# Kernel tuning notes

Hardware: AMD Instinct MI355X
Metric: run time of the kernel (lower is better)

The kernel has to match this reference:

```python
import jax, jax.numpy as jnp
import numpy as np

N_HEAD = 16
ROPE_CACHE = 2500  # Rotary module caches tables of length 2500
NEG_INF = -1e30


def _rope_tables(head_dim):
    inv_freq = 1.0 / (10000.0 ** (jnp.arange(0, head_dim, 2, dtype=jnp.float32) / head_dim))
    t = jnp.arange(ROPE_CACHE, dtype=jnp.float32)
    freqs = t[:, None] * inv_freq[None, :]            # (2500, head_dim//2)
    emb = jnp.concatenate([freqs, freqs], axis=-1)    # (2500, head_dim)
    return jnp.cos(emb), jnp.sin(emb)


def _rotate_half(x):
    h = x.shape[-1] // 2
    return jnp.concatenate([-x[..., h:], x[..., :h]], axis=-1)


def setup_inputs() -> dict:
    key = jax.random.key(0)
    ks = jax.random.split(key, 8)
    B, S, D = 2, 2048, 1024
    H = N_HEAD
    hd = D // H
    return {
        "qx": jax.random.normal(ks[0], (B, S, D), jnp.float32),
        "kvx": jax.random.normal(ks[1], (B, S, D), jnp.float32),
        "k_cache": jnp.zeros((B, H, S, hd), jnp.float32),
        "v_cache": jnp.zeros((B, H, S, hd), jnp.float32),
        "Wq": jax.random.normal(ks[2], (D, D), jnp.float32) * 0.02,
        "bq": jnp.zeros((D,), jnp.float32),
        "Wk": jax.random.normal(ks[3], (D, D), jnp.float32) * 0.02,
        "Wv": jax.random.normal(ks[4], (D, D), jnp.float32) * 0.02,
        "bv": jnp.zeros((D,), jnp.float32),
        "Wo": jax.random.normal(ks[5], (D, D), jnp.float32) * 0.02,
        "bo": jnp.zeros((D,), jnp.float32),
        "q_positions": jnp.arange(S, dtype=jnp.int32),
        "kv_positions": jnp.arange(S, dtype=jnp.int32),
    }


def reference(qx, kvx, k_cache, v_cache, Wq, bq, Wk, Wv, bv, Wo, bo, q_positions, kv_positions):
    B, Sq, D = qx.shape
    H = N_HEAD
    hd = D // H
    Skv = kvx.shape[1]
    cos, sin = _rope_tables(hd)
    # sqrt_qk_scale = sqrt(1) = 1, folded out.

    def rope(x, pos):  # x: (B, S, H, hd)
        c = cos[pos][None, :, None, :]
        s = sin[pos][None, :, None, :]
        return x * c + _rotate_half(x) * s

    # projections (torch Linear: y = x @ W.T + b; key has no bias)
    q = (qx @ Wq.T + bq).reshape(B, Sq, H, hd)
    q = rope(q, q_positions).transpose(0, 2, 1, 3)            # (B,H,Sq,hd)
    k = (kvx @ Wk.T).reshape(B, Skv, H, hd)
    k = rope(k, kv_positions).transpose(0, 2, 1, 3)           # (B,H,Skv,hd)
    v = (kvx @ Wv.T + bv).reshape(B, Skv, H, hd).transpose(0, 2, 1, 3)

    # KV-cache scatter update: k_cache[:, :, kv_positions] = k
    k_cache = k_cache.at[:, :, kv_positions].set(k)
    v_cache = v_cache.at[:, :, kv_positions].set(v)
    Sc = k_cache.shape[2]

    # SDPA (causal), scaled by 1/sqrt(head_dim) as in F.scaled_dot_product_attention
    scores = jnp.einsum('bhqd,bhkd->bhqk', q, k_cache) / jnp.sqrt(jnp.float32(hd))
    causal = jnp.arange(Sq)[:, None] >= jnp.arange(Sc)[None, :]
    scores = jnp.where(causal[None, None], scores, NEG_INF)
    attn = jax.nn.softmax(scores, axis=-1)
    wv = jnp.einsum('bhqk,bhkd->bhqd', attn, v_cache)

    out = wv.transpose(0, 2, 1, 3).reshape(B, Sq, D) @ Wo.T + bo
    return out
```

## Files before the change

### kernel.cpp

```cpp
#include <hip/hip_runtime.h>
#include <cstdint>
#include <cstddef>

#define NH   16
#define SEQ  2048
#define DM   1024
#define HD   64
#define KDIM 1024
#define MROWS 4096
#define CH   2

using short8  = __attribute__((ext_vector_type(8))) short;
using short4v = __attribute__((ext_vector_type(4))) short;
using floatx4 = __attribute__((ext_vector_type(4))) float;

__device__ __forceinline__ short f2bf(float f) {
  unsigned int u = __float_as_uint(f);
  u += 0x7fffu + ((u >> 16) & 1u);
  return (short)(u >> 16);
}
__device__ __forceinline__ float bf2f(short s) {
  return __uint_as_float(((unsigned int)(unsigned short)s) << 16);
}

__device__ __forceinline__ void async_ld16(const void* g, void* l) {
  __builtin_amdgcn_global_load_lds(
      (const __attribute__((address_space(1))) void*)g,
      (__attribute__((address_space(3))) void*)l, 16, 0, 0);
}

struct Cvt6 { const float* src[6]; short* dst[6]; int n[6]; };

__global__ void convert6(Cvt6 a) {
  const int which = blockIdx.y;
  const float4* s = (const float4*)a.src[which];
  short4v* d = (short4v*)a.dst[which];
  const int n4 = a.n[which] >> 2;
  const int stride = gridDim.x * blockDim.x;
  for (int i = blockIdx.x * blockDim.x + threadIdx.x; i < n4; i += stride) {
    float4 v = s[i];
    short4v o;
    o.x = f2bf(v.x); o.y = f2bf(v.y); o.z = f2bf(v.z); o.w = f2bf(v.w);
    d[i] = o;
  }
}

__device__ __forceinline__ void gemm_core(const short* __restrict__ A,
                                          const short* __restrict__ B,
                                          int row0, int col0,
                                          short* As, short* Bs,
                                          floatx4 (&acc)[4][4], int tid) {
  const int lane = tid & 63;
  const int w = tid >> 6;
  const int quad = lane >> 4;
  const int ln = lane & 15;
  const int wr = w >> 1, wc = w & 1;

  int rr[2], cc[2];
#pragma unroll
  for (int g = 0; g < 2; ++g) {
    int beta = (w + 4 * g) * 1024 + lane * 16;
    rr[g] = beta >> 6;
    cc[g] = (beta & 63) >> 1;
  }
#pragma unroll
  for (int i = 0; i < 4; ++i)
#pragma unroll
    for (int j = 0; j < 4; ++j) acc[i][j] = (floatx4){0.f, 0.f, 0.f, 0.f};

  for (int k0 = 0; k0 < KDIM; k0 += 32) {
    __syncthreads();
#pragma unroll
    for (int g = 0; g < 2; ++g) {
      async_ld16(A + (size_t)(row0 + rr[g]) * KDIM + k0 + cc[g], As + (w + 4 * g) * 512);
      async_ld16(B + (size_t)(col0 + rr[g]) * KDIM + k0 + cc[g], Bs + (w + 4 * g) * 512);
    }
    __syncthreads();

    short8 af[4], bfr[4];
#pragma unroll
    for (int i = 0; i < 4; ++i)
      af[i] = *(const short8*)(As + (wr * 64 + i * 16 + ln) * 32 + quad * 8);
#pragma unroll
    for (int j = 0; j < 4; ++j)
      bfr[j] = *(const short8*)(Bs + (wc * 64 + j * 16 + ln) * 32 + quad * 8);
#pragma unroll
    for (int i = 0; i < 4; ++i)
#pragma unroll
      for (int j = 0; j < 4; ++j)
        acc[i][j] = __builtin_amdgcn_mfma_f32_16x16x32_bf16(af[i], bfr[j], acc[i][j], 0, 0, 0);
  }
}

__global__ __launch_bounds__(256) void proj_gemm(
    const short* __restrict__ qxb, const short* __restrict__ kvxb,
    const short* __restrict__ Wqb, const short* __restrict__ Wkb,
    const short* __restrict__ Wvb,
    const float* __restrict__ bq, const float* __restrict__ bv,
    short* __restrict__ Qo, short* __restrict__ Ko, short* __restrict__ Vt,
    const int* __restrict__ qpos, const int* __restrict__ kvpos) {
  __shared__ __align__(16) short As[128 * 32];
  __shared__ __align__(16) short Bs[128 * 32];

  const int tid = threadIdx.x;
  const int lane = tid & 63;
  const int w = tid >> 6;
  const int quad = lane >> 4;
  const int ln = lane & 15;
  const int wr = w >> 1, wc = w & 1;
  const int z = blockIdx.z;

  int row0, col0;
  const short *A, *B;
  if (z == 2) {
    A = Wvb; B = kvxb;
    row0 = blockIdx.x * 128;
    col0 = blockIdx.y * 128;
  } else {
    A = z ? kvxb : qxb;
    B = z ? Wkb : Wqb;
    row0 = blockIdx.y * 128;
    col0 = blockIdx.x * 128;
  }

  floatx4 acc[4][4];
  gemm_core(A, B, row0, col0, As, Bs, acc, tid);

  if (z == 2) {
#pragma unroll
    for (int i = 0; i < 4; ++i)
#pragma unroll
      for (int r = 0; r < 4; ++r) {
        int nr = row0 + wr * 64 + i * 16 + quad * 4 + r;
        int h = nr >> 6, d = nr & 63;
        float bb = bv[nr];
        size_t base = ((size_t)(h)*HD + d) * SEQ;
#pragma unroll
        for (int j = 0; j < 4; ++j) {
          int sc = col0 + wc * 64 + j * 16 + ln;
          int b = sc >> 11, s = sc & (SEQ - 1);
          Vt[((size_t)b * NH * HD) * SEQ + base + s] = f2bf(acc[i][j][r] + bb);
        }
      }
  } else {
    const int colbase = col0 + wc * 64;
    const float scale = (z == 0) ? 0.125f : 1.0f;
    const float* bias = (z == 0) ? bq : nullptr;
    const int* pos = (z == 0) ? qpos : kvpos;
    short* Out = (z == 0) ? Qo : Ko;
#pragma unroll
    for (int j = 0; j < 2; ++j) {
      int col1 = colbase + j * 16 + ln;
      float b1 = bias ? bias[col1] : 0.f;
      float b2 = bias ? bias[col1 + 32] : 0.f;
      int h = col1 >> 6;
      int d1 = col1 & 63;
      float fr = __powf(10000.f, -(float)d1 * (1.f / 32.f));
#pragma unroll
      for (int i = 0; i < 4; ++i)
#pragma unroll
        for (int r = 0; r < 4; ++r) {
          int row = row0 + wr * 64 + i * 16 + quad * 4 + r;
          int b = row >> 11, s = row & (SEQ - 1);
          float ang = (float)pos[s] * fr;
          float sn, cs;
          __sincosf(ang, &sn, &cs);
          float x1 = acc[i][j][r] + b1;
          float x2 = acc[i][j + 2][r] + b2;
          float o1 = (x1 * cs - x2 * sn) * scale;
          float o2 = (x2 * cs + x1 * sn) * scale;
          size_t basq = ((((size_t)b * NH + h) * SEQ) + s) * HD;
          Out[basq + d1] = f2bf(o1);
          Out[basq + d1 + 32] = f2bf(o2);
        }
    }
  }
}

__global__ __launch_bounds__(256) void out_gemm(
    const short* __restrict__ Ab, const short* __restrict__ Bb,
    const float* __restrict__ bias, float* __restrict__ out) {
  __shared__ __align__(16) short As[128 * 32];
  __shared__ __align__(16) short Bs[128 * 32];
  const int tid = threadIdx.x;
  const int lane = tid & 63;
  const int w = tid >> 6;
  const int quad = lane >> 4;
  const int ln = lane & 15;
  const int wr = w >> 1, wc = w & 1;
  const int row0 = blockIdx.y * 128;
  const int col0 = blockIdx.x * 128;

  floatx4 acc[4][4];
  gemm_core(Ab, Bb, row0, col0, As, Bs, acc, tid);

#pragma unroll
  for (int j = 0; j < 4; ++j) {
    int col = col0 + wc * 64 + j * 16 + ln;
    float bb = bias[col];
#pragma unroll
    for (int i = 0; i < 4; ++i)
#pragma unroll
      for (int r = 0; r < 4; ++r) {
        int row = row0 + wr * 64 + i * 16 + quad * 4 + r;
        out[(size_t)row * DM + col] = acc[i][j][r] + bb;
      }
  }
}

__global__ __launch_bounds__(128) void attn_partial(
    const short* __restrict__ Q, const short* __restrict__ Kc,
    const short* __restrict__ Vtg, short* __restrict__ Po,
    float* __restrict__ Lo) {
  const int tid = threadIdx.x;
  const int lane = tid & 63;
  const int w = tid >> 6;
  const int quad = lane >> 4;
  const int ln = lane & 15;
  const int bh = blockIdx.y;
  const int bx = blockIdx.x;
  const int qt = 31 - (bx >> 1);
  const int ch = bx & (CH - 1);
  if (ch > qt) return;

  const int q0 = qt * 64;
  const int wlo = q0 + w * 32;

  const short* Qb = Q + (size_t)bh * SEQ * HD;
  const short* Kb = Kc + (size_t)bh * SEQ * HD;
  const short* Vb = Vtg + (size_t)bh * HD * SEQ;

  __shared__ __align__(16) short Ks[2 * 64 * 32];
  __shared__ __align__(16) short Vs[2 * 64 * 32];
  __shared__ __align__(16) short Pt[2][32 * 72];

  short8 qa[2][2];
#pragma unroll
  for (int i = 0; i < 2; ++i)
#pragma unroll
    for (int kk = 0; kk < 2; ++kk)
      qa[i][kk] = *(const short8*)(Qb + (size_t)(wlo + i * 16 + ln) * HD +
                                   quad * 8 + kk * 32);

  floatx4 oacc[4][2];
  float lp[2];
#pragma unroll
  for (int jd = 0; jd < 4; ++jd)
#pragma unroll
    for (int i = 0; i < 2; ++i) oacc[jd][i] = (floatx4){0.f, 0.f, 0.f, 0.f};
  lp[0] = lp[1] = 0.f;

  for (int t = ch * 64; t <= q0; t += CH * 64) {
    __syncthreads();
#pragma unroll
    for (int g = 0; g < 4; ++g) {
      int slot = (w * 4 + g) * 64 + lane;
      int kk = slot >> 8, rowi = (slot >> 2) & 63, grp = slot & 3;
      async_ld16(Kb + (size_t)(t + rowi) * HD + kk * 32 + grp * 8,
                 (char*)Ks + slot * 16);
      async_ld16(Vb + (size_t)rowi * SEQ + t + kk * 32 + grp * 8,
                 (char*)Vs + slot * 16);
    }
    __syncthreads();

    floatx4 sacc[4][2];
#pragma unroll
    for (int c = 0; c < 4; ++c)
#pragma unroll
      for (int i = 0; i < 2; ++i) sacc[c][i] = (floatx4){0.f, 0.f, 0.f, 0.f};
#pragma unroll
    for (int kk = 0; kk < 2; ++kk)
#pragma unroll
      for (int c = 0; c < 4; ++c) {
        short8 kb = *(const short8*)(Ks + kk * 2048 + (c * 16 + ln) * 32 + quad * 8);
        sacc[c][0] = __builtin_amdgcn_mfma_f32_16x16x32_bf16(kb, qa[0][kk], sacc[c][0], 0, 0, 0);
        sacc[c][1] = __builtin_amdgcn_mfma_f32_16x16x32_bf16(kb, qa[1][kk], sacc[c][1], 0, 0, 0);
      }

    const bool dmask = (t == q0);
#pragma unroll
    for (int c = 0; c < 4; ++c)
#pragma unroll
      for (int i = 0; i < 2; ++i) {
        short4v pk;
#pragma unroll
        for (int r = 0; r < 4; ++r) {
          float p = __expf(sacc[c][i][r]);
          if (dmask) {
            int sp = t + c * 16 + quad * 4 + r;
            int qq = wlo + i * 16 + ln;
            if (sp > qq) p = 0.f;
          }
          lp[i] += p;
          pk[r] = f2bf(p);
        }
        *(short4v*)(&Pt[w][(i * 16 + ln) * 72 + c * 16 + quad * 4]) = pk;
      }

#pragma unroll
    for (int kk = 0; kk < 2; ++kk) {
      short8 pb0 = *(const short8*)(&Pt[w][(ln) * 72 + kk * 32 + quad * 8]);
      short8 pb1 = *(const short8*)(&Pt[w][(16 + ln) * 72 + kk * 32 + quad * 8]);
#pragma unroll
      for (int jd = 0; jd < 4; ++jd) {
        short8 va = *(const short8*)(Vs + kk * 2048 + (jd * 16 + ln) * 32 + quad * 8);
        oacc[jd][0] = __builtin_amdgcn_mfma_f32_16x16x32_bf16(va, pb0, oacc[jd][0], 0, 0, 0);
        oacc[jd][1] = __builtin_amdgcn_mfma_f32_16x16x32_bf16(va, pb1, oacc[jd][1], 0, 0, 0);
      }
    }
  }

  const size_t idx = ((size_t)bh * 32 + qt) * CH + ch;
  short* Pob = Po + idx * 4096;
#pragma unroll
  for (int jd = 0; jd < 4; ++jd)
#pragma unroll
    for (int i = 0; i < 2; ++i) {
      short4v pk;
#pragma unroll
      for (int r = 0; r < 4; ++r) pk[r] = f2bf(oacc[jd][i][r]);
      *(short4v*)(Pob + (w * 32 + i * 16 + ln) * 64 + jd * 16 + quad * 4) = pk;
    }
#pragma unroll
  for (int i = 0; i < 2; ++i) {
    float l = lp[i];
    l += __shfl_xor(l, 16, 64);
    l += __shfl_xor(l, 32, 64);
    if (quad == 0) Lo[idx * 64 + w * 32 + i * 16 + ln] = l;
  }
}

__global__ __launch_bounds__(256) void attn_reduce(
    const short* __restrict__ Po, const float* __restrict__ Lo,
    short* __restrict__ Ov) {
  const int qt = blockIdx.x;
  const int bh = blockIdx.y;
  const int b = bh >> 4, h = bh & 15;
  const int tid = threadIdx.x;
  const int ql = tid >> 2;
  const int d0 = (tid & 3) * 16;
  const int nch = (qt >= 1) ? CH : 1;
  const size_t i0 = ((size_t)bh * 32 + qt) * CH;

  float l = Lo[i0 * 64 + ql];
  const short8* p0 = (const short8*)(Po + i0 * 4096 + ql * 64 + d0);
  short8 a0 = p0[0], a1 = p0[1];
  float acc[16];
#pragma unroll
  for (int e = 0; e < 8; ++e) { acc[e] = bf2f(a0[e]); acc[8 + e] = bf2f(a1[e]); }
  if (nch == 2) {
    l += Lo[(i0 + 1) * 64 + ql];
    const short8* p1 = (const short8*)(Po + (i0 + 1) * 4096 + ql * 64 + d0);
    short8 c0 = p1[0], c1 = p1[1];
#pragma unroll
    for (int e = 0; e < 8; ++e) { acc[e] += bf2f(c0[e]); acc[8 + e] += bf2f(c1[e]); }
  }
  float inv = 1.f / l;
  short8 o0, o1;
#pragma unroll
  for (int e = 0; e < 8; ++e) { o0[e] = f2bf(acc[e] * inv); o1[e] = f2bf(acc[8 + e] * inv); }
  int s = qt * 64 + ql;
  short* dst = Ov + ((size_t)b * SEQ + s) * DM + h * HD + d0;
  *(short8*)dst = o0;
  *((short8*)dst + 1) = o1;
}

extern "C" void kernel_launch(void* const* d_in, const int* in_sizes, int n_in,
                              void* d_out, int out_size, void* d_ws, size_t ws_size,
                              hipStream_t stream) {
  const float* qx  = (const float*)d_in[0];
  const float* kvx = (const float*)d_in[1];
  const float* Wq = (const float*)d_in[4];
  const float* bq = (const float*)d_in[5];
  const float* Wk = (const float*)d_in[6];
  const float* Wv = (const float*)d_in[7];
  const float* bv = (const float*)d_in[8];
  const float* Wo = (const float*)d_in[9];
  const float* bo = (const float*)d_in[10];
  const int* qpos  = (const int*)d_in[11];
  const int* kvpos = (const int*)d_in[12];

  char* ws = (char*)d_ws;
  short* qxb  = (short*)(ws + 0);
  short* kvxb = (short*)(ws + 8388608);
  short* Wqb  = (short*)(ws + 16777216);
  short* Wkb  = (short*)(ws + 18874368);
  short* Wvb  = (short*)(ws + 20971520);
  short* Wob  = (short*)(ws + 23068672);
  short* Qbf  = (short*)(ws + 25165824);
  short* Kbf  = (short*)(ws + 33554432);
  short* Vtb  = (short*)(ws + 41943040);
  short* WVbf = (short*)(ws + 50331648);
  short* Po = (short*)(ws + 0);
  float* Lo = (float*)(ws + 16777216);

  Cvt6 c;
  c.src[0] = qx;  c.dst[0] = qxb;  c.n[0] = MROWS * KDIM;
  c.src[1] = kvx; c.dst[1] = kvxb; c.n[1] = MROWS * KDIM;
  c.src[2] = Wq;  c.dst[2] = Wqb;  c.n[2] = DM * KDIM;
  c.src[3] = Wk;  c.dst[3] = Wkb;  c.n[3] = DM * KDIM;
  c.src[4] = Wv;  c.dst[4] = Wvb;  c.n[4] = DM * KDIM;
  c.src[5] = Wo;  c.dst[5] = Wob;  c.n[5] = DM * KDIM;
  convert6<<<dim3(1024, 6), 256, 0, stream>>>(c);

  proj_gemm<<<dim3(DM / 128, MROWS / 128, 3), 256, 0, stream>>>(
      qxb, kvxb, Wqb, Wkb, Wvb, bq, bv, Qbf, Kbf, Vtb, qpos, kvpos);

  attn_partial<<<dim3(32 * CH, 2 * NH), 128, 0, stream>>>(Qbf, Kbf, Vtb, Po, Lo);

  attn_reduce<<<dim3(SEQ / 64, 2 * NH), 256, 0, stream>>>(Po, Lo, WVbf);

  out_gemm<<<dim3(DM / 128, MROWS / 128), 256, 0, stream>>>(
      WVbf, Wob, bo, (float*)d_out);
}
```

Before: 265.6 us.

## Precompute RoPE tables, deepen GEMM K-tile, split attention across four waves

Three independent changes. The converter kernel now also builds cos/sin tables per position, so the projection epilogue reads them from memory instead of calling powf and sincos per element. The shared GEMM core loads 64-wide K slices per step, halving the number of barriers and loop iterations at the cost of twice the LDS. Attention blocks now use 256 threads with 16 query rows per wave instead of 128 threads with 32, which adds wavefronts per block but lowers per-wave MFMA reuse of K/V fragments.

```diff
diff --git a/kernel.cpp b/kernel.cpp
--- a/kernel.cpp
+++ b/kernel.cpp
@@ -29,19 +29,38 @@
       (__attribute__((address_space(3))) void*)l, 16, 0, 0);
 }
 
-struct Cvt6 { const float* src[6]; short* dst[6]; int n[6]; };
-
-__global__ void convert6(Cvt6 a) {
+struct Cvt8 {
+  const float* src[8];
+  void* dst[8];
+  int n[8];
+  const int* pos[8];
+};
+
+__global__ void convert8(Cvt8 a) {
   const int which = blockIdx.y;
-  const float4* s = (const float4*)a.src[which];
-  short4v* d = (short4v*)a.dst[which];
-  const int n4 = a.n[which] >> 2;
   const int stride = gridDim.x * blockDim.x;
-  for (int i = blockIdx.x * blockDim.x + threadIdx.x; i < n4; i += stride) {
-    float4 v = s[i];
-    short4v o;
-    o.x = f2bf(v.x); o.y = f2bf(v.y); o.z = f2bf(v.z); o.w = f2bf(v.w);
-    d[i] = o;
+  if (which < 6) {
+    const float4* s = (const float4*)a.src[which];
+    short4v* d = (short4v*)a.dst[which];
+    const int n4 = a.n[which] >> 2;
+    for (int i = blockIdx.x * blockDim.x + threadIdx.x; i < n4; i += stride) {
+      float4 v = s[i];
+      short4v o;
+      o.x = f2bf(v.x); o.y = f2bf(v.y); o.z = f2bf(v.z); o.w = f2bf(v.w);
+      d[i] = o;
+    }
+  } else {
+    const int* pos = a.pos[which];
+    float2* d = (float2*)a.dst[which];
+    const int n = a.n[which];
+    for (int i = blockIdx.x * blockDim.x + threadIdx.x; i < n; i += stride) {
+      int s = i >> 5, d1 = i & 31;
+      float fr = __powf(10000.f, -(float)d1 * (1.f / 32.f));
+      float ang = (float)pos[s] * fr;
+      float sn, cs;
+      __sincosf(ang, &sn, &cs);
+      d[i] = make_float2(cs, sn);
+    }
   }
 }
 
@@ -56,39 +75,45 @@
   const int ln = lane & 15;
   const int wr = w >> 1, wc = w & 1;
 
-  int rr[2], cc[2];
-#pragma unroll
-  for (int g = 0; g < 2; ++g) {
-    int beta = (w + 4 * g) * 1024 + lane * 16;
-    rr[g] = beta >> 6;
-    cc[g] = (beta & 63) >> 1;
+  int kks[4], rws[4], grs[4];
+#pragma unroll
+  for (int g = 0; g < 4; ++g) {
+    int slot = (w * 4 + g) * 64 + lane;
+    kks[g] = slot >> 9;
+    rws[g] = (slot >> 2) & 127;
+    grs[g] = slot & 3;
   }
 #pragma unroll
   for (int i = 0; i < 4; ++i)
 #pragma unroll
     for (int j = 0; j < 4; ++j) acc[i][j] = (floatx4){0.f, 0.f, 0.f, 0.f};
 
-  for (int k0 = 0; k0 < KDIM; k0 += 32) {
+  for (int k0 = 0; k0 < KDIM; k0 += 64) {
     __syncthreads();
 #pragma unroll
-    for (int g = 0; g < 2; ++g) {
-      async_ld16(A + (size_t)(row0 + rr[g]) * KDIM + k0 + cc[g], As + (w + 4 * g) * 512);
-      async_ld16(B + (size_t)(col0 + rr[g]) * KDIM + k0 + cc[g], Bs + (w + 4 * g) * 512);
+    for (int g = 0; g < 4; ++g) {
+      int slot = (w * 4 + g) * 64 + lane;
+      int src = k0 + kks[g] * 32 + grs[g] * 8;
+      async_ld16(A + (size_t)(row0 + rws[g]) * KDIM + src, As + slot * 8);
+      async_ld16(B + (size_t)(col0 + rws[g]) * KDIM + src, Bs + slot * 8);
     }
     __syncthreads();
 
-    short8 af[4], bfr[4];
-#pragma unroll
-    for (int i = 0; i < 4; ++i)
-      af[i] = *(const short8*)(As + (wr * 64 + i * 16 + ln) * 32 + quad * 8);
-#pragma unroll
-    for (int j = 0; j < 4; ++j)
-      bfr[j] = *(const short8*)(Bs + (wc * 64 + j * 16 + ln) * 32 + quad * 8);
-#pragma unroll
-    for (int i = 0; i < 4; ++i)
+#pragma unroll
+    for (int ks = 0; ks < 2; ++ks) {
+      short8 af[4], bfr[4];
+#pragma unroll
+      for (int i = 0; i < 4; ++i)
+        af[i] = *(const short8*)(As + ks * 4096 + (wr * 64 + i * 16 + ln) * 32 + quad * 8);
 #pragma unroll
       for (int j = 0; j < 4; ++j)
-        acc[i][j] = __builtin_amdgcn_mfma_f32_16x16x32_bf16(af[i], bfr[j], acc[i][j], 0, 0, 0);
+        bfr[j] = *(const short8*)(Bs + ks * 4096 + (wc * 64 + j * 16 + ln) * 32 + quad * 8);
+#pragma unroll
+      for (int i = 0; i < 4; ++i)
+#pragma unroll
+        for (int j = 0; j < 4; ++j)
+          acc[i][j] = __builtin_amdgcn_mfma_f32_16x16x32_bf16(af[i], bfr[j], acc[i][j], 0, 0, 0);
+    }
   }
 }
 
@@ -98,9 +123,9 @@
     const short* __restrict__ Wvb,
     const float* __restrict__ bq, const float* __restrict__ bv,
     short* __restrict__ Qo, short* __restrict__ Ko, short* __restrict__ Vt,
-    const int* __restrict__ qpos, const int* __restrict__ kvpos) {
-  __shared__ __align__(16) short As[128 * 32];
-  __shared__ __align__(16) short Bs[128 * 32];
+    const float2* __restrict__ qtab, const float2* __restrict__ ktab) {
+  __shared__ __align__(16) short As[128 * 64];
+  __shared__ __align__(16) short Bs[128 * 64];
 
   const int tid = threadIdx.x;
   const int lane = tid & 63;
@@ -146,7 +171,7 @@
     const int colbase = col0 + wc * 64;
     const float scale = (z == 0) ? 0.125f : 1.0f;
     const float* bias = (z == 0) ? bq : nullptr;
-    const int* pos = (z == 0) ? qpos : kvpos;
+    const float2* tab = (z == 0) ? qtab : ktab;
     short* Out = (z == 0) ? Qo : Ko;
 #pragma unroll
     for (int j = 0; j < 2; ++j) {
@@ -155,20 +180,17 @@
       float b2 = bias ? bias[col1 + 32] : 0.f;
       int h = col1 >> 6;
       int d1 = col1 & 63;
-      float fr = __powf(10000.f, -(float)d1 * (1.f / 32.f));
 #pragma unroll
       for (int i = 0; i < 4; ++i)
 #pragma unroll
         for (int r = 0; r < 4; ++r) {
           int row = row0 + wr * 64 + i * 16 + quad * 4 + r;
           int b = row >> 11, s = row & (SEQ - 1);
-          float ang = (float)pos[s] * fr;
-          float sn, cs;
-          __sincosf(ang, &sn, &cs);
+          float2 cs_sn = tab[s * 32 + d1];
           float x1 = acc[i][j][r] + b1;
           float x2 = acc[i][j + 2][r] + b2;
-          float o1 = (x1 * cs - x2 * sn) * scale;
-          float o2 = (x2 * cs + x1 * sn) * scale;
+          float o1 = (x1 * cs_sn.x - x2 * cs_sn.y) * scale;
+          float o2 = (x2 * cs_sn.x + x1 * cs_sn.y) * scale;
           size_t basq = ((((size_t)b * NH + h) * SEQ) + s) * HD;
           Out[basq + d1] = f2bf(o1);
           Out[basq + d1 + 32] = f2bf(o2);
@@ -180,8 +202,8 @@
 __global__ __launch_bounds__(256) void out_gemm(
     const short* __restrict__ Ab, const short* __restrict__ Bb,
     const float* __restrict__ bias, float* __restrict__ out) {
-  __shared__ __align__(16) short As[128 * 32];
-  __shared__ __align__(16) short Bs[128 * 32];
+  __shared__ __align__(16) short As[128 * 64];
+  __shared__ __align__(16) short Bs[128 * 64];
   const int tid = threadIdx.x;
   const int lane = tid & 63;
   const int w = tid >> 6;
@@ -208,7 +230,7 @@
   }
 }
 
-__global__ __launch_bounds__(128) void attn_partial(
+__global__ __launch_bounds__(256) void attn_partial(
     const short* __restrict__ Q, const short* __restrict__ Kc,
     const short* __restrict__ Vtg, short* __restrict__ Po,
     float* __restrict__ Lo) {
@@ -224,7 +246,7 @@
   if (ch > qt) return;
 
   const int q0 = qt * 64;
-  const int wlo = q0 + w * 32;
+  const int wlo = q0 + w * 16;
 
   const short* Qb = Q + (size_t)bh * SEQ * HD;
   const short* Kb = Kc + (size_t)bh * SEQ * HD;
@@ -232,29 +254,23 @@
 
   __shared__ __align__(16) short Ks[2 * 64 * 32];
   __shared__ __align__(16) short Vs[2 * 64 * 32];
-  __shared__ __align__(16) short Pt[2][32 * 72];
-
-  short8 qa[2][2];
-#pragma unroll
-  for (int i = 0; i < 2; ++i)
-#pragma unroll
-    for (int kk = 0; kk < 2; ++kk)
-      qa[i][kk] = *(const short8*)(Qb + (size_t)(wlo + i * 16 + ln) * HD +
-                                   quad * 8 + kk * 32);
-
-  floatx4 oacc[4][2];
-  float lp[2];
-#pragma unroll
-  for (int jd = 0; jd < 4; ++jd)
-#pragma unroll
-    for (int i = 0; i < 2; ++i) oacc[jd][i] = (floatx4){0.f, 0.f, 0.f, 0.f};
-  lp[0] = lp[1] = 0.f;
+  __shared__ __align__(16) short Pt[4][16 * 72];
+
+  short8 qa[2];
+#pragma unroll
+  for (int kk = 0; kk < 2; ++kk)
+    qa[kk] = *(const short8*)(Qb + (size_t)(wlo + ln) * HD + quad * 8 + kk * 32);
+
+  floatx4 oacc[4];
+  float lp = 0.f;
+#pragma unroll
+  for (int jd = 0; jd < 4; ++jd) oacc[jd] = (floatx4){0.f, 0.f, 0.f, 0.f};
 
   for (int t = ch * 64; t <= q0; t += CH * 64) {
     __syncthreads();
 #pragma unroll
-    for (int g = 0; g < 4; ++g) {
-      int slot = (w * 4 + g) * 64 + lane;
+    for (int g = 0; g < 2; ++g) {
+      int slot = (w * 2 + g) * 64 + lane;
       int kk = slot >> 8, rowi = (slot >> 2) & 63, grp = slot & 3;
       async_ld16(Kb + (size_t)(t + rowi) * HD + kk * 32 + grp * 8,
                  (char*)Ks + slot * 16);
@@ -263,49 +279,42 @@
     }
     __syncthreads();
 
-    floatx4 sacc[4][2];
-#pragma unroll
-    for (int c = 0; c < 4; ++c)
-#pragma unroll
-      for (int i = 0; i < 2; ++i) sacc[c][i] = (floatx4){0.f, 0.f, 0.f, 0.f};
+    floatx4 sacc[4];
+#pragma unroll
+    for (int c = 0; c < 4; ++c) sacc[c] = (floatx4){0.f, 0.f, 0.f, 0.f};
 #pragma unroll
     for (int kk = 0; kk < 2; ++kk)
 #pragma unroll
       for (int c = 0; c < 4; ++c) {
         short8 kb = *(const short8*)(Ks + kk * 2048 + (c * 16 + ln) * 32 + quad * 8);
-        sacc[c][0] = __builtin_amdgcn_mfma_f32_16x16x32_bf16(kb, qa[0][kk], sacc[c][0], 0, 0, 0);
-        sacc[c][1] = __builtin_amdgcn_mfma_f32_16x16x32_bf16(kb, qa[1][kk], sacc[c][1], 0, 0, 0);
+        sacc[c] = __builtin_amdgcn_mfma_f32_16x16x32_bf16(kb, qa[kk], sacc[c], 0, 0, 0);
       }
 
     const bool dmask = (t == q0);
 #pragma unroll
-    for (int c = 0; c < 4; ++c)
-#pragma unroll
-      for (int i = 0; i < 2; ++i) {
-        short4v pk;
-#pragma unroll
-        for (int r = 0; r < 4; ++r) {
-          float p = __expf(sacc[c][i][r]);
-          if (dmask) {
-            int sp = t + c * 16 + quad * 4 + r;
-            int qq = wlo + i * 16 + ln;
-            if (sp > qq) p = 0.f;
-          }
-          lp[i] += p;
-          pk[r] = f2bf(p);
+    for (int c = 0; c < 4; ++c) {
+      short4v pk;
+#pragma unroll
+      for (int r = 0; r < 4; ++r) {
+        float p = __expf(sacc[c][r]);
+        if (dmask) {
+          int sp = t + c * 16 + quad * 4 + r;
+          int qq = wlo + ln;
+          if (sp > qq) p = 0.f;
         }
-        *(short4v*)(&Pt[w][(i * 16 + ln) * 72 + c * 16 + quad * 4]) = pk;
+        lp += p;
+        pk[r] = f2bf(p);
       }
+      *(short4v*)(&Pt[w][ln * 72 + c * 16 + quad * 4]) = pk;
+    }
 
 #pragma unroll
     for (int kk = 0; kk < 2; ++kk) {
-      short8 pb0 = *(const short8*)(&Pt[w][(ln) * 72 + kk * 32 + quad * 8]);
-      short8 pb1 = *(const short8*)(&Pt[w][(16 + ln) * 72 + kk * 32 + quad * 8]);
+      short8 pb = *(const short8*)(&Pt[w][ln * 72 + kk * 32 + quad * 8]);
 #pragma unroll
       for (int jd = 0; jd < 4; ++jd) {
         short8 va = *(const short8*)(Vs + kk * 2048 + (jd * 16 + ln) * 32 + quad * 8);
-        oacc[jd][0] = __builtin_amdgcn_mfma_f32_16x16x32_bf16(va, pb0, oacc[jd][0], 0, 0, 0);
-        oacc[jd][1] = __builtin_amdgcn_mfma_f32_16x16x32_bf16(va, pb1, oacc[jd][1], 0, 0, 0);
+        oacc[jd] = __builtin_amdgcn_mfma_f32_16x16x32_bf16(va, pb, oacc[jd], 0, 0, 0);
       }
     }
   }
@@ -313,21 +322,16 @@
   const size_t idx = ((size_t)bh * 32 + qt) * CH + ch;
   short* Pob = Po + idx * 4096;
 #pragma unroll
-  for (int jd = 0; jd < 4; ++jd)
-#pragma unroll
-    for (int i = 0; i < 2; ++i) {
-      short4v pk;
-#pragma unroll
-      for (int r = 0; r < 4; ++r) pk[r] = f2bf(oacc[jd][i][r]);
-      *(short4v*)(Pob + (w * 32 + i * 16 + ln) * 64 + jd * 16 + quad * 4) = pk;
-    }
-#pragma unroll
-  for (int i = 0; i < 2; ++i) {
-    float l = lp[i];
-    l += __shfl_xor(l, 16, 64);
-    l += __shfl_xor(l, 32, 64);
-    if (quad == 0) Lo[idx * 64 + w * 32 + i * 16 + ln] = l;
-  }
+  for (int jd = 0; jd < 4; ++jd) {
+    short4v pk;
+#pragma unroll
+    for (int r = 0; r < 4; ++r) pk[r] = f2bf(oacc[jd][r]);
+    *(short4v*)(Pob + (w * 16 + ln) * 64 + jd * 16 + quad * 4) = pk;
+  }
+  float l = lp;
+  l += __shfl_xor(l, 16, 64);
+  l += __shfl_xor(l, 32, 64);
+  if (quad == 0) Lo[idx * 64 + w * 16 + ln] = l;
 }
 
 __global__ __launch_bounds__(256) void attn_reduce(
@@ -391,22 +395,26 @@
   short* Kbf  = (short*)(ws + 33554432);
   short* Vtb  = (short*)(ws + 41943040);
   short* WVbf = (short*)(ws + 50331648);
+  float2* qtab = (float2*)(ws + 50331648);
+  float2* ktab = (float2*)(ws + 50331648 + 524288);
   short* Po = (short*)(ws + 0);
   float* Lo = (float*)(ws + 16777216);
 
-  Cvt6 c;
-  c.src[0] = qx;  c.dst[0] = qxb;  c.n[0] = MROWS * KDIM;
-  c.src[1] = kvx; c.dst[1] = kvxb; c.n[1] = MROWS * KDIM;
-  c.src[2] = Wq;  c.dst[2] = Wqb;  c.n[2] = DM * KDIM;
-  c.src[3] = Wk;  c.dst[3] = Wkb;  c.n[3] = DM * KDIM;
-  c.src[4] = Wv;  c.dst[4] = Wvb;  c.n[4] = DM * KDIM;
-  c.src[5] = Wo;  c.dst[5] = Wob;  c.n[5] = DM * KDIM;
-  convert6<<<dim3(1024, 6), 256, 0, stream>>>(c);
+  Cvt8 c;
+  c.src[0] = qx;  c.dst[0] = qxb;  c.n[0] = MROWS * KDIM; c.pos[0] = nullptr;
+  c.src[1] = kvx; c.dst[1] = kvxb; c.n[1] = MROWS * KDIM; c.pos[1] = nullptr;
+  c.src[2] = Wq;  c.dst[2] = Wqb;  c.n[2] = DM * KDIM;    c.pos[2] = nullptr;
+  c.src[3] = Wk;  c.dst[3] = Wkb;  c.n[3] = DM * KDIM;    c.pos[3] = nullptr;
+  c.src[4] = Wv;  c.dst[4] = Wvb;  c.n[4] = DM * KDIM;    c.pos[4] = nullptr;
+  c.src[5] = Wo;  c.dst[5] = Wob;  c.n[5] = DM * KDIM;    c.pos[5] = nullptr;
+  c.src[6] = nullptr; c.dst[6] = qtab; c.n[6] = SEQ * 32; c.pos[6] = qpos;
+  c.src[7] = nullptr; c.dst[7] = ktab; c.n[7] = SEQ * 32; c.pos[7] = kvpos;
+  convert8<<<dim3(1024, 8), 256, 0, stream>>>(c);
 
   proj_gemm<<<dim3(DM / 128, MROWS / 128, 3), 256, 0, stream>>>(
-      qxb, kvxb, Wqb, Wkb, Wvb, bq, bv, Qbf, Kbf, Vtb, qpos, kvpos);
-
-  attn_partial<<<dim3(32 * CH, 2 * NH), 128, 0, stream>>>(Qbf, Kbf, Vtb, Po, Lo);
+      qxb, kvxb, Wqb, Wkb, Wvb, bq, bv, Qbf, Kbf, Vtb, qtab, ktab);
+
+  attn_partial<<<dim3(32 * CH, 2 * NH), 256, 0, stream>>>(Qbf, Kbf, Vtb, Po, Lo);
 
   attn_reduce<<<dim3(SEQ / 64, 2 * NH), 256, 0, stream>>>(Po, Lo, WVbf);
 
```

After: 264.9 us. About the same (-0.3%).
